# Kernel optimization log

Hardware: AMD Instinct MI355X
Metric: run time of the kernel (lower is better)

The kernel has to match this reference:

```python
import jax, jax.numpy as jnp
import numpy as np

N_NODES = 100000
IN_CH, HID_CH, OUT_CH = 128, 256, 128
N_EDGES = 1600000
N_LABEL = 200000


def setup_inputs() -> dict:
    key = jax.random.key(0)
    ks = jax.random.split(key, 9)
    x = jax.random.normal(ks[0], (N_NODES, IN_CH), dtype=jnp.float32)
    edge_index = jax.random.randint(ks[1], (2, N_EDGES), 0, N_NODES, dtype=jnp.int64)
    edge_label_index = jax.random.randint(ks[2], (2, N_LABEL), 0, N_NODES, dtype=jnp.int64)
    def glorot(k, fan_in, fan_out):
        s = jnp.sqrt(2.0 / (fan_in + fan_out))
        return jax.random.normal(k, (fan_in, fan_out), dtype=jnp.float32) * s
    # SAGEConv params: lin_l (aggregated neighbors, with bias), lin_r (root, no bias)
    Wl1 = glorot(ks[3], IN_CH, HID_CH)
    bl1 = jnp.zeros((HID_CH,), dtype=jnp.float32)
    Wr1 = glorot(ks[4], IN_CH, HID_CH)
    Wl2 = glorot(ks[5], HID_CH, OUT_CH)
    bl2 = jnp.zeros((OUT_CH,), dtype=jnp.float32)
    Wr2 = glorot(ks[6], HID_CH, OUT_CH)
    return {"x": x, "edge_index": edge_index, "edge_label_index": edge_label_index,
            "Wl1": Wl1, "bl1": bl1, "Wr1": Wr1, "Wl2": Wl2, "bl2": bl2, "Wr2": Wr2}


def _sage_conv(x, src, dst, Wl, bl, Wr):
    # mean aggregation of source-node messages onto destination nodes
    n = x.shape[0]
    agg = jax.ops.segment_sum(x[src], dst, num_segments=n)          # [N, d]
    deg = jax.ops.segment_sum(jnp.ones_like(dst, dtype=x.dtype), dst, num_segments=n)
    agg = agg / jnp.maximum(deg, 1.0)[:, None]
    return agg @ Wl + bl + x @ Wr


def reference(x, edge_index, edge_label_index, Wl1, bl1, Wr1, Wl2, bl2, Wr2):
    src, dst = edge_index[0], edge_index[1]
    h = jax.nn.relu(_sage_conv(x, src, dst, Wl1, bl1, Wr1))
    z = _sage_conv(h, src, dst, Wl2, bl2, Wr2)                      # [N, out]
    lsrc, ldst = edge_label_index[0], edge_label_index[1]
    return jnp.sum(z[lsrc] * z[ldst], axis=-1)                      # [E_label]
```

## Files before the change

### kernel.cpp

```cpp
#include <hip/hip_runtime.h>

#define N_NODES 100000
#define N_EDGES 1600000
#define N_LABEL 200000
#define C_IN 128
#define C_HID 256
#define C_OUT 128

#define BCHUNK 64
#define NBUCK ((N_NODES + BCHUNK - 1) / BCHUNK)
#define NBF 64
#define EPB (N_EDGES / NBF)
#define FLEN (NBUCK * NBF)
#define ESTORE 2048

typedef __attribute__((ext_vector_type(8))) short bf16x8;
typedef __attribute__((ext_vector_type(4))) float f32x4;

__device__ __forceinline__ ushort f2bf(float f) {
  uint u = __float_as_uint(f);
  return (ushort)((u + 0x7fffu + ((u >> 16) & 1u)) >> 16);
}

__device__ __forceinline__ float bfl(uint u) { return __uint_as_float(u << 16); }
__device__ __forceinline__ float bfh(uint u) {
  return __uint_as_float(u & 0xffff0000u);
}

__device__ __forceinline__ void async_copy16(const void* g, void* lds) {
  __builtin_amdgcn_global_load_lds((const __attribute__((address_space(1))) void*)g,
                                   (__attribute__((address_space(3))) void*)lds,
                                   16, 0, 0);
}

__global__ __launch_bounds__(256) void bucket_count(const int* __restrict__ dst,
                                                    int* __restrict__ cnt) {
  __shared__ int lcnt[NBUCK];
  const int t = threadIdx.x;
  const int base = blockIdx.x * EPB;
  for (int b = t; b < NBUCK; b += 256) lcnt[b] = 0;
  __syncthreads();
  for (int i = t; i < EPB; i += 256) {
    atomicAdd(&lcnt[dst[base + i] >> 6], 1);
  }
  __syncthreads();
  for (int b = t; b < NBUCK; b += 256) cnt[b * NBF + blockIdx.x] = lcnt[b];
}

template <int LEN>
__global__ __launch_bounds__(256) void scan_sums(const int* __restrict__ a,
                                                 int* __restrict__ bsum) {
  __shared__ int red[256];
  const int t = threadIdx.x;
  const int idx = blockIdx.x * 1024 + t * 4;
  int s = 0;
  if (idx + 3 < LEN) {
    const int4 v = *(const int4*)&a[idx];
    s = v.x + v.y + v.z + v.w;
  } else {
    for (int j = 0; j < 4 && idx + j < LEN; ++j) s += a[idx + j];
  }
  red[t] = s;
  __syncthreads();
  for (int off = 128; off > 0; off >>= 1) {
    if (t < off) red[t] += red[t + off];
    __syncthreads();
  }
  if (t == 0) bsum[blockIdx.x] = red[0];
}

__global__ __launch_bounds__(128) void scan_tops(const int* __restrict__ bsum,
                                                 int* __restrict__ bpre,
                                                 int* __restrict__ total, int nb) {
  __shared__ int sh[128];
  const int t = threadIdx.x;
  sh[t] = (t < nb) ? bsum[t] : 0;
  __syncthreads();
  for (int off = 1; off < 128; off <<= 1) {
    int v = 0;
    if (t >= off) v = sh[t - off];
    __syncthreads();
    if (t >= off) sh[t] += v;
    __syncthreads();
  }
  if (t < nb) bpre[t] = (t == 0) ? 0 : sh[t - 1];
  if (t == nb - 1) *total = sh[t];
}

template <int LEN>
__global__ __launch_bounds__(256) void scan_apply(int* __restrict__ a,
                                                  const int* __restrict__ bpre) {
  __shared__ int sh[256];
  const int t = threadIdx.x;
  const int idx = blockIdx.x * 1024 + t * 4;
  int4 v = make_int4(0, 0, 0, 0);
  const bool full = (idx + 3 < LEN);
  if (full) {
    v = *(const int4*)&a[idx];
  } else {
    if (idx + 0 < LEN) v.x = a[idx + 0];
    if (idx + 1 < LEN) v.y = a[idx + 1];
    if (idx + 2 < LEN) v.z = a[idx + 2];
    if (idx + 3 < LEN) v.w = a[idx + 3];
  }
  sh[t] = v.x + v.y + v.z + v.w;
  __syncthreads();
  for (int off = 1; off < 256; off <<= 1) {
    int u = 0;
    if (t >= off) u = sh[t - off];
    __syncthreads();
    if (t >= off) sh[t] += u;
    __syncthreads();
  }
  const int base = bpre[blockIdx.x] + ((t == 0) ? 0 : sh[t - 1]);
  int4 e;
  e.x = base;
  e.y = base + v.x;
  e.z = base + v.x + v.y;
  e.w = base + v.x + v.y + v.z;
  if (full) {
    *(int4*)&a[idx] = e;
  } else {
    if (idx + 0 < LEN) a[idx + 0] = e.x;
    if (idx + 1 < LEN) a[idx + 1] = e.y;
    if (idx + 2 < LEN) a[idx + 2] = e.z;
    if (idx + 3 < LEN) a[idx + 3] = e.w;
  }
}

__global__ __launch_bounds__(256) void bucket_fill(const int* __restrict__ src,
                                                   const int* __restrict__ dst,
                                                   const int* __restrict__ cnt,
                                                   uint* __restrict__ tmp) {
  __shared__ int lcur[NBUCK];
  const int t = threadIdx.x;
  const int base = blockIdx.x * EPB;
  for (int b = t; b < NBUCK; b += 256) lcur[b] = cnt[b * NBF + blockIdx.x];
  __syncthreads();
  for (int i = t; i < EPB; i += 256) {
    const int d = dst[base + i];
    const int s = src[base + i];
    const int pos = atomicAdd(&lcur[d >> 6], 1);
    tmp[pos] = ((uint)s << 6) | (uint)(d & 63);
  }
}

__global__ __launch_bounds__(256) void csr_build(const int* __restrict__ cnt,
                                                 uint* __restrict__ tmp,
                                                 int* __restrict__ row_start) {
  __shared__ uint est[ESTORE];
  __shared__ uint eso[ESTORE];
  __shared__ int lcnt[BCHUNK];
  __shared__ int lcur[BCHUNK];
  const int b = blockIdx.x;
  const int t = threadIdx.x;
  const int s = cnt[b * NBF];
  const int e = cnt[(b + 1) * NBF];
  const int n = e - s;
  for (int j = t; j < n; j += 256) est[j] = tmp[s + j];
  if (t < BCHUNK) lcnt[t] = 0;
  __syncthreads();
  for (int j = t; j < n; j += 256) atomicAdd(&lcnt[est[j] & 63], 1);
  __syncthreads();
  for (int off = 1; off < BCHUNK; off <<= 1) {
    int v = 0;
    if (t >= off && t < BCHUNK) v = lcnt[t - off];
    __syncthreads();
    if (t >= off && t < BCHUNK) lcnt[t] += v;
    __syncthreads();
  }
  if (t < BCHUNK) {
    const int ex = (t == 0) ? 0 : lcnt[t - 1];
    lcur[t] = ex;
    const int node = b * BCHUNK + t;
    if (node < N_NODES) row_start[node] = s + ex;
  }
  if (b == NBUCK - 1 && t == 0) row_start[N_NODES] = e;
  __syncthreads();
  for (int j = t; j < n; j += 256) {
    const uint v = est[j];
    const int pos = atomicAdd(&lcur[v & 63], 1);
    eso[pos] = v >> 6;
  }
  __syncthreads();
  for (int j = t; j < n; j += 256) tmp[s + j] = eso[j];
}

__global__ __launch_bounds__(256) void cast_bf16(const float* __restrict__ in,
                                                 ushort* __restrict__ out) {
  const size_t i = ((size_t)blockIdx.x * 256 + threadIdx.x) * 8;
  const float4 a = *(const float4*)&in[i];
  const float4 b = *(const float4*)&in[i + 4];
  uint4 o;
  o.x = (uint)f2bf(a.x) | ((uint)f2bf(a.y) << 16);
  o.y = (uint)f2bf(a.z) | ((uint)f2bf(a.w) << 16);
  o.z = (uint)f2bf(b.x) | ((uint)f2bf(b.y) << 16);
  o.w = (uint)f2bf(b.z) | ((uint)f2bf(b.w) << 16);
  *(uint4*)&out[i] = o;
}

__global__ __launch_bounds__(256) void prep_wt(const float* __restrict__ Wl1,
                                               const float* __restrict__ Wr1,
                                               const float* __restrict__ Wl2,
                                               const float* __restrict__ Wr2,
                                               ushort* __restrict__ WT1,
                                               ushort* __restrict__ WT2) {
  const int n = blockIdx.x;
  const int k = threadIdx.x;
  const float v1 = (k < 128) ? Wl1[k * 256 + n] : Wr1[(k - 128) * 256 + n];
  WT1[n * 256 + k] = f2bf(v1);
  const float v2 = (n < 128) ? Wl2[k * 128 + n] : Wr2[k * 128 + (n - 128)];
  WT2[n * 256 + k] = f2bf(v2);
}

template <int MODE>
__global__ __launch_bounds__(256) void gather_mean_b(const int* __restrict__ row_start,
                                                     const uint* __restrict__ csr_src,
                                                     const ushort* __restrict__ feat,
                                                     ushort* __restrict__ bout,
                                                     float* __restrict__ z) {
  const int wid = blockIdx.x * 4 + (threadIdx.x >> 6);
  const int lane = threadIdx.x & 63;
  if (wid >= N_NODES) return;
  const int s = row_start[wid];
  const int e = row_start[wid + 1];
  const int slot = lane >> 4;
  const int c0 = (lane & 15) * 8;
  float acc[8] = {};
  int j = s + slot;
#define ACC8(r)                                   \
  acc[0] += bfl(r.x); acc[1] += bfh(r.x);         \
  acc[2] += bfl(r.y); acc[3] += bfh(r.y);         \
  acc[4] += bfl(r.z); acc[5] += bfh(r.z);         \
  acc[6] += bfl(r.w); acc[7] += bfh(r.w);
  for (; j + 12 < e; j += 16) {
    const uint s0 = csr_src[j];
    const uint s1 = csr_src[j + 4];
    const uint s2 = csr_src[j + 8];
    const uint s3 = csr_src[j + 12];
    const uint4 r0 = *(const uint4*)&feat[(size_t)s0 * 128 + c0];
    const uint4 r1 = *(const uint4*)&feat[(size_t)s1 * 128 + c0];
    const uint4 r2 = *(const uint4*)&feat[(size_t)s2 * 128 + c0];
    const uint4 r3 = *(const uint4*)&feat[(size_t)s3 * 128 + c0];
    ACC8(r0) ACC8(r1) ACC8(r2) ACC8(r3)
  }
  for (; j < e; j += 4) {
    const uint s0 = csr_src[j];
    const uint4 r0 = *(const uint4*)&feat[(size_t)s0 * 128 + c0];
    ACC8(r0)
  }
#undef ACC8
#pragma unroll
  for (int k = 0; k < 8; ++k) {
    acc[k] += __shfl_xor(acc[k], 16, 64);
    acc[k] += __shfl_xor(acc[k], 32, 64);
  }
  if (slot == 0) {
    const float rd = 1.0f / fmaxf((float)(e - s), 1.0f);
    if (MODE == 0) {
      uint4 o;
      o.x = (uint)f2bf(acc[0] * rd) | ((uint)f2bf(acc[1] * rd) << 16);
      o.y = (uint)f2bf(acc[2] * rd) | ((uint)f2bf(acc[3] * rd) << 16);
      o.z = (uint)f2bf(acc[4] * rd) | ((uint)f2bf(acc[5] * rd) << 16);
      o.w = (uint)f2bf(acc[6] * rd) | ((uint)f2bf(acc[7] * rd) << 16);
      *(uint4*)&bout[(size_t)wid * 128 + c0] = o;
    } else {
      float4 z0 = *(const float4*)&z[(size_t)wid * 128 + c0];
      float4 z1 = *(const float4*)&z[(size_t)wid * 128 + c0 + 4];
      z0.x += acc[0] * rd; z0.y += acc[1] * rd;
      z0.z += acc[2] * rd; z0.w += acc[3] * rd;
      z1.x += acc[4] * rd; z1.y += acc[5] * rd;
      z1.z += acc[6] * rd; z1.w += acc[7] * rd;
      *(float4*)&z[(size_t)wid * 128 + c0] = z0;
      *(float4*)&z[(size_t)wid * 128 + c0 + 4] = z1;
    }
  }
}

__global__ __launch_bounds__(256) void gemm_fused(const ushort* __restrict__ aggb,
                                                  const ushort* __restrict__ xb,
                                                  const ushort* __restrict__ WT1,
                                                  const ushort* __restrict__ WT2,
                                                  const float* __restrict__ bl1,
                                                  const float* __restrict__ bl2,
                                                  ushort* __restrict__ p,
                                                  float* __restrict__ zp) {
  __shared__ ushort As[2][2048];
  __shared__ ushort Bs[2][8192];
  __shared__ ushort Ht[64 * 256];
  const int tid = threadIdx.x;
  const int w = tid >> 6;
  const int l = tid & 63;
  const int row0 = blockIdx.x * 64;
  const int wn = w * 64;
  const int fr = l & 15;
  const int kg16 = (l >> 4) * 16;
  const int cr = (l >> 4) * 4;
  const int cc = l & 15;

  const int arow = tid >> 2;
  const int akb = (tid & 3) * 16;
  const int akbs = akb ^ (((arow >> 1) & 3) << 4);
  int agr = row0 + arow;
  agr = (agr < N_NODES) ? agr : (N_NODES - 1);
  const int brow_l = l >> 2;
  const int bkb = (l & 3) * 16;

#define STAGE(buf, kc)                                                        \
  {                                                                           \
    const ushort* Ab_ = ((kc) < 4) ? aggb : xb;                               \
    async_copy16((const char*)Ab_ + (size_t)agr * 256 + ((kc)&3) * 64 + akbs, \
                 (char*)As[buf] + w * 1024);                                  \
    _Pragma("unroll") for (int i_ = 0; i_ < 4; ++i_) {                        \
      const int c_ = w * 4 + i_;                                              \
      const int n_ = c_ * 16 + brow_l;                                        \
      const int kbs_ = bkb ^ (((n_ >> 1) & 3) << 4);                          \
      async_copy16((const char*)WT1 + (size_t)n_ * 512 + (kc)*64 + kbs_,      \
                   (char*)Bs[buf] + c_ * 1024);                               \
    }                                                                         \
  }

  {
    f32x4 acc[4][4] = {};
    STAGE(0, 0)
    __syncthreads();
    int cur = 0;
#pragma unroll
    for (int kc = 0; kc < 8; ++kc) {
      if (kc < 7) STAGE(cur ^ 1, kc + 1)
      bf16x8 af[4], bfr[4];
#pragma unroll
      for (int i = 0; i < 4; ++i) {
        const int ra = i * 16 + fr;
        const int ba = ra * 64 + (kg16 ^ (((ra >> 1) & 3) << 4));
        af[i] = *(const bf16x8*)((const char*)As[cur] + ba);
      }
#pragma unroll
      for (int j = 0; j < 4; ++j) {
        const int nb = wn + j * 16 + fr;
        const int bb = nb * 64 + (kg16 ^ (((nb >> 1) & 3) << 4));
        bfr[j] = *(const bf16x8*)((const char*)Bs[cur] + bb);
      }
#pragma unroll
      for (int i = 0; i < 4; ++i)
#pragma unroll
        for (int j = 0; j < 4; ++j)
          acc[i][j] = __builtin_amdgcn_mfma_f32_16x16x32_bf16(af[i], bfr[j],
                                                              acc[i][j], 0, 0, 0);
      __syncthreads();
      cur ^= 1;
    }
#pragma unroll
    for (int i = 0; i < 4; ++i) {
#pragma unroll
      for (int j = 0; j < 4; ++j) {
        const int col = wn + j * 16 + cc;
        const float bv = bl1[col];
#pragma unroll
        for (int r = 0; r < 4; ++r) {
          const int row = i * 16 + cr + r;
          const float v = fmaxf(acc[i][j][r] + bv, 0.f);
          const int ba = (row * 512 + col * 2) ^ ((row & 7) << 4);
          *(ushort*)((char*)Ht + ba) = f2bf(v);
        }
      }
    }
  }
#undef STAGE
  __syncthreads();

  f32x4 acc2[4][4] = {};
#pragma unroll
  for (int kc = 0; kc < 8; ++kc) {
    bf16x8 af[4], bfr[4];
#pragma unroll
    for (int i = 0; i < 4; ++i) {
      const int row = i * 16 + fr;
      const int ba = (row * 512 + kc * 64 + kg16) ^ ((row & 7) << 4);
      af[i] = *(const bf16x8*)((const char*)Ht + ba);
    }
#pragma unroll
    for (int j = 0; j < 4; ++j) {
      const int n = wn + j * 16 + fr;
      bfr[j] = *(const bf16x8*)((const char*)WT2 + (size_t)n * 512 + kc * 64 +
                                kg16);
    }
#pragma unroll
    for (int i = 0; i < 4; ++i)
#pragma unroll
      for (int j = 0; j < 4; ++j)
        acc2[i][j] = __builtin_amdgcn_mfma_f32_16x16x32_bf16(af[i], bfr[j],
                                                             acc2[i][j], 0, 0, 0);
  }
#pragma unroll
  for (int i = 0; i < 4; ++i) {
#pragma unroll
    for (int j = 0; j < 4; ++j) {
      const int col = wn + j * 16 + cc;
      const int gcl = col & 127;
      const bool is_p = (col < 128);
      const float bv = is_p ? 0.f : bl2[gcl];
#pragma unroll
      for (int r = 0; r < 4; ++r) {
        const int grow = row0 + i * 16 + cr + r;
        if (grow < N_NODES) {
          const float v = acc2[i][j][r] + bv;
          if (is_p)
            p[(size_t)grow * 128 + gcl] = f2bf(v);
          else
            zp[(size_t)grow * 128 + gcl] = v;
        }
      }
    }
  }
}

__global__ __launch_bounds__(256) void dot_kernel(const int* __restrict__ ls,
                                                  const int* __restrict__ ld,
                                                  const float* __restrict__ z,
                                                  float* __restrict__ out) {
  long long tid = (long long)blockIdx.x * 256 + threadIdx.x;
  int e = (int)(tid >> 5);
  int lane = (int)(tid & 31);
  if (e >= N_LABEL) return;
  int a = ls[e], b = ld[e];
  const float4 va = *(const float4*)&z[(size_t)a * 128 + lane * 4];
  const float4 vb = *(const float4*)&z[(size_t)b * 128 + lane * 4];
  float p = va.x * vb.x + va.y * vb.y + va.z * vb.z + va.w * vb.w;
  p += __shfl_xor(p, 16, 32);
  p += __shfl_xor(p, 8, 32);
  p += __shfl_xor(p, 4, 32);
  p += __shfl_xor(p, 2, 32);
  p += __shfl_xor(p, 1, 32);
  if (lane == 0) out[e] = p;
}

extern "C" void kernel_launch(void* const* d_in, const int* in_sizes, int n_in,
                              void* d_out, int out_size, void* d_ws, size_t ws_size,
                              hipStream_t stream) {
  const float* x = (const float*)d_in[0];
  const int* ei = (const int*)d_in[1];
  const int* eli = (const int*)d_in[2];
  const float* Wl1 = (const float*)d_in[3];
  const float* bl1 = (const float*)d_in[4];
  const float* Wr1 = (const float*)d_in[5];
  const float* Wl2 = (const float*)d_in[6];
  const float* bl2 = (const float*)d_in[7];
  const float* Wr2 = (const float*)d_in[8];
  float* out = (float*)d_out;

  const int* e_src = ei;
  const int* e_dst = ei + N_EDGES;
  const int* l_src = eli;
  const int* l_dst = eli + N_LABEL;

  char* ws = (char*)d_ws;
  ushort* xb = (ushort*)(ws + 0);
  ushort* aggb = (ushort*)(ws + 25600000);
  ushort* p = (ushort*)(ws + 102400000);
  float* z = (float*)(ws + 128000000);
  ushort* WT1 = (ushort*)(ws + 179200000);
  ushort* WT2 = (ushort*)(ws + 179331072);
  uint* tmp = (uint*)(ws + 179462144);
  int* cnt = (int*)(ws + 185862144);
  int* bsum = (int*)(ws + 186270000);
  int* bpre = bsum + 128;
  int* row_start = (int*)(ws + 186280000);

  const int SBLK = (FLEN + 1023) / 1024;

  bucket_count<<<NBF, 256, 0, stream>>>(e_dst, cnt);
  scan_sums<FLEN><<<SBLK, 256, 0, stream>>>(cnt, bsum);
  scan_tops<<<1, 128, 0, stream>>>(bsum, bpre, &cnt[FLEN], SBLK);
  scan_apply<FLEN><<<SBLK, 256, 0, stream>>>(cnt, bpre);
  bucket_fill<<<NBF, 256, 0, stream>>>(e_src, e_dst, cnt, tmp);
  csr_build<<<NBUCK, 256, 0, stream>>>(cnt, tmp, row_start);

  cast_bf16<<<(N_NODES * C_IN) / (256 * 8), 256, 0, stream>>>(x, xb);
  prep_wt<<<256, 256, 0, stream>>>(Wl1, Wr1, Wl2, Wr2, WT1, WT2);

  gather_mean_b<0><<<(N_NODES + 3) / 4, 256, 0, stream>>>(row_start, tmp, xb,
                                                          aggb, nullptr);
  gemm_fused<<<(N_NODES + 63) / 64, 256, 0, stream>>>(aggb, xb, WT1, WT2, bl1,
                                                      bl2, p, z);
  gather_mean_b<1><<<(N_NODES + 3) / 4, 256, 0, stream>>>(row_start, tmp, p,
                                                          nullptr, z);

  dot_kernel<<<(int)(((long long)N_LABEL * 32) / 256), 256, 0, stream>>>(
      l_src, l_dst, z, out);
}
```

Measured before the change: 348.0 us.

## Merge prep kernels, fold scan tops into apply, single-buffer GEMM staging

```diff
diff --git a/kernel.cpp b/kernel.cpp
--- a/kernel.cpp
+++ b/kernel.cpp
@@ -13,6 +13,8 @@
 #define EPB (N_EDGES / NBF)
 #define FLEN (NBUCK * NBF)
 #define ESTORE 2048
+#define CAST_NB ((N_NODES * C_IN) / (256 * 8))
+#define SBLK ((FLEN + 1023) / 1024)
 
 typedef __attribute__((ext_vector_type(8))) short bf16x8;
 typedef __attribute__((ext_vector_type(4))) float f32x4;
@@ -33,32 +35,59 @@
                                    16, 0, 0);
 }
 
-__global__ __launch_bounds__(256) void bucket_count(const int* __restrict__ dst,
-                                                    int* __restrict__ cnt) {
+__global__ __launch_bounds__(256) void prep_kernel(const int* __restrict__ dst,
+                                                   int* __restrict__ cnt,
+                                                   const float* __restrict__ Wl1,
+                                                   const float* __restrict__ Wr1,
+                                                   const float* __restrict__ Wl2,
+                                                   const float* __restrict__ Wr2,
+                                                   ushort* __restrict__ WT1,
+                                                   ushort* __restrict__ WT2,
+                                                   const float* __restrict__ x,
+                                                   ushort* __restrict__ xb) {
   __shared__ int lcnt[NBUCK];
+  const int blk = blockIdx.x;
   const int t = threadIdx.x;
-  const int base = blockIdx.x * EPB;
-  for (int b = t; b < NBUCK; b += 256) lcnt[b] = 0;
-  __syncthreads();
-  for (int i = t; i < EPB; i += 256) {
-    atomicAdd(&lcnt[dst[base + i] >> 6], 1);
-  }
-  __syncthreads();
-  for (int b = t; b < NBUCK; b += 256) cnt[b * NBF + blockIdx.x] = lcnt[b];
-}
-
-template <int LEN>
+  if (blk < NBF) {
+    const int base = blk * EPB;
+    for (int b = t; b < NBUCK; b += 256) lcnt[b] = 0;
+    __syncthreads();
+    for (int i = t; i < EPB; i += 256) {
+      atomicAdd(&lcnt[dst[base + i] >> 6], 1);
+    }
+    __syncthreads();
+    for (int b = t; b < NBUCK; b += 256) cnt[b * NBF + blk] = lcnt[b];
+  } else if (blk < NBF + 256) {
+    const int n = blk - NBF;
+    const int k = t;
+    const float v1 = (k < 128) ? Wl1[k * 256 + n] : Wr1[(k - 128) * 256 + n];
+    WT1[n * 256 + k] = f2bf(v1);
+    const float v2 = (n < 128) ? Wl2[k * 128 + n] : Wr2[k * 128 + (n - 128)];
+    WT2[n * 256 + k] = f2bf(v2);
+  } else {
+    const size_t i = ((size_t)(blk - NBF - 256) * 256 + t) * 8;
+    const float4 a = *(const float4*)&x[i];
+    const float4 b = *(const float4*)&x[i + 4];
+    uint4 o;
+    o.x = (uint)f2bf(a.x) | ((uint)f2bf(a.y) << 16);
+    o.y = (uint)f2bf(a.z) | ((uint)f2bf(a.w) << 16);
+    o.z = (uint)f2bf(b.x) | ((uint)f2bf(b.y) << 16);
+    o.w = (uint)f2bf(b.z) | ((uint)f2bf(b.w) << 16);
+    *(uint4*)&xb[i] = o;
+  }
+}
+
 __global__ __launch_bounds__(256) void scan_sums(const int* __restrict__ a,
                                                  int* __restrict__ bsum) {
   __shared__ int red[256];
   const int t = threadIdx.x;
   const int idx = blockIdx.x * 1024 + t * 4;
   int s = 0;
-  if (idx + 3 < LEN) {
+  if (idx + 3 < FLEN) {
     const int4 v = *(const int4*)&a[idx];
     s = v.x + v.y + v.z + v.w;
   } else {
-    for (int j = 0; j < 4 && idx + j < LEN; ++j) s += a[idx + j];
+    for (int j = 0; j < 4 && idx + j < FLEN; ++j) s += a[idx + j];
   }
   red[t] = s;
   __syncthreads();
@@ -69,39 +98,33 @@
   if (t == 0) bsum[blockIdx.x] = red[0];
 }
 
-__global__ __launch_bounds__(128) void scan_tops(const int* __restrict__ bsum,
-                                                 int* __restrict__ bpre,
-                                                 int* __restrict__ total, int nb) {
-  __shared__ int sh[128];
+__global__ __launch_bounds__(256) void scan_apply(int* __restrict__ a,
+                                                  const int* __restrict__ bsum) {
+  __shared__ int sh[256];
+  __shared__ int bsc[128];
   const int t = threadIdx.x;
-  sh[t] = (t < nb) ? bsum[t] : 0;
+  if (t < 128) bsc[t] = (t < SBLK) ? bsum[t] : 0;
   __syncthreads();
   for (int off = 1; off < 128; off <<= 1) {
     int v = 0;
-    if (t >= off) v = sh[t - off];
-    __syncthreads();
-    if (t >= off) sh[t] += v;
-    __syncthreads();
-  }
-  if (t < nb) bpre[t] = (t == 0) ? 0 : sh[t - 1];
-  if (t == nb - 1) *total = sh[t];
-}
-
-template <int LEN>
-__global__ __launch_bounds__(256) void scan_apply(int* __restrict__ a,
-                                                  const int* __restrict__ bpre) {
-  __shared__ int sh[256];
-  const int t = threadIdx.x;
+    if (t < 128 && t >= off) v = bsc[t - off];
+    __syncthreads();
+    if (t < 128 && t >= off) bsc[t] += v;
+    __syncthreads();
+  }
+  const int bbase = (blockIdx.x == 0) ? 0 : bsc[blockIdx.x - 1];
+  if (blockIdx.x == SBLK - 1 && t == 0) a[FLEN] = bsc[SBLK - 1];
+
   const int idx = blockIdx.x * 1024 + t * 4;
   int4 v = make_int4(0, 0, 0, 0);
-  const bool full = (idx + 3 < LEN);
+  const bool full = (idx + 3 < FLEN);
   if (full) {
     v = *(const int4*)&a[idx];
   } else {
-    if (idx + 0 < LEN) v.x = a[idx + 0];
-    if (idx + 1 < LEN) v.y = a[idx + 1];
-    if (idx + 2 < LEN) v.z = a[idx + 2];
-    if (idx + 3 < LEN) v.w = a[idx + 3];
+    if (idx + 0 < FLEN) v.x = a[idx + 0];
+    if (idx + 1 < FLEN) v.y = a[idx + 1];
+    if (idx + 2 < FLEN) v.z = a[idx + 2];
+    if (idx + 3 < FLEN) v.w = a[idx + 3];
   }
   sh[t] = v.x + v.y + v.z + v.w;
   __syncthreads();
@@ -112,7 +135,7 @@
     if (t >= off) sh[t] += u;
     __syncthreads();
   }
-  const int base = bpre[blockIdx.x] + ((t == 0) ? 0 : sh[t - 1]);
+  const int base = bbase + ((t == 0) ? 0 : sh[t - 1]);
   int4 e;
   e.x = base;
   e.y = base + v.x;
@@ -121,10 +144,10 @@
   if (full) {
     *(int4*)&a[idx] = e;
   } else {
-    if (idx + 0 < LEN) a[idx + 0] = e.x;
-    if (idx + 1 < LEN) a[idx + 1] = e.y;
-    if (idx + 2 < LEN) a[idx + 2] = e.z;
-    if (idx + 3 < LEN) a[idx + 3] = e.w;
+    if (idx + 0 < FLEN) a[idx + 0] = e.x;
+    if (idx + 1 < FLEN) a[idx + 1] = e.y;
+    if (idx + 2 < FLEN) a[idx + 2] = e.z;
+    if (idx + 3 < FLEN) a[idx + 3] = e.w;
   }
 }
 
@@ -184,33 +207,6 @@
   }
   __syncthreads();
   for (int j = t; j < n; j += 256) tmp[s + j] = eso[j];
-}
-
-__global__ __launch_bounds__(256) void cast_bf16(const float* __restrict__ in,
-                                                 ushort* __restrict__ out) {
-  const size_t i = ((size_t)blockIdx.x * 256 + threadIdx.x) * 8;
-  const float4 a = *(const float4*)&in[i];
-  const float4 b = *(const float4*)&in[i + 4];
-  uint4 o;
-  o.x = (uint)f2bf(a.x) | ((uint)f2bf(a.y) << 16);
-  o.y = (uint)f2bf(a.z) | ((uint)f2bf(a.w) << 16);
-  o.z = (uint)f2bf(b.x) | ((uint)f2bf(b.y) << 16);
-  o.w = (uint)f2bf(b.z) | ((uint)f2bf(b.w) << 16);
-  *(uint4*)&out[i] = o;
-}
-
-__global__ __launch_bounds__(256) void prep_wt(const float* __restrict__ Wl1,
-                                               const float* __restrict__ Wr1,
-                                               const float* __restrict__ Wl2,
-                                               const float* __restrict__ Wr2,
-                                               ushort* __restrict__ WT1,
-                                               ushort* __restrict__ WT2) {
-  const int n = blockIdx.x;
-  const int k = threadIdx.x;
-  const float v1 = (k < 128) ? Wl1[k * 256 + n] : Wr1[(k - 128) * 256 + n];
-  WT1[n * 256 + k] = f2bf(v1);
-  const float v2 = (n < 128) ? Wl2[k * 128 + n] : Wr2[k * 128 + (n - 128)];
-  WT2[n * 256 + k] = f2bf(v2);
 }
 
 template <int MODE>
@@ -285,8 +281,8 @@
                                                   const float* __restrict__ bl2,
                                                   ushort* __restrict__ p,
                                                   float* __restrict__ zp) {
-  __shared__ ushort As[2][2048];
-  __shared__ ushort Bs[2][8192];
+  __shared__ ushort As[2048];
+  __shared__ ushort Bs[8192];
   __shared__ ushort Ht[64 * 256];
   const int tid = threadIdx.x;
   const int w = tid >> 6;
@@ -306,40 +302,34 @@
   const int brow_l = l >> 2;
   const int bkb = (l & 3) * 16;
 
-#define STAGE(buf, kc)                                                        \
-  {                                                                           \
-    const ushort* Ab_ = ((kc) < 4) ? aggb : xb;                               \
-    async_copy16((const char*)Ab_ + (size_t)agr * 256 + ((kc)&3) * 64 + akbs, \
-                 (char*)As[buf] + w * 1024);                                  \
-    _Pragma("unroll") for (int i_ = 0; i_ < 4; ++i_) {                        \
-      const int c_ = w * 4 + i_;                                              \
-      const int n_ = c_ * 16 + brow_l;                                        \
-      const int kbs_ = bkb ^ (((n_ >> 1) & 3) << 4);                          \
-      async_copy16((const char*)WT1 + (size_t)n_ * 512 + (kc)*64 + kbs_,      \
-                   (char*)Bs[buf] + c_ * 1024);                               \
-    }                                                                         \
-  }
-
   {
     f32x4 acc[4][4] = {};
-    STAGE(0, 0)
-    __syncthreads();
-    int cur = 0;
-#pragma unroll
     for (int kc = 0; kc < 8; ++kc) {
-      if (kc < 7) STAGE(cur ^ 1, kc + 1)
+      const ushort* Ab = (kc < 4) ? aggb : xb;
+      __syncthreads();
+      async_copy16((const char*)Ab + (size_t)agr * 256 + (kc & 3) * 64 + akbs,
+                   (char*)As + w * 1024);
+#pragma unroll
+      for (int i_ = 0; i_ < 4; ++i_) {
+        const int c_ = w * 4 + i_;
+        const int n_ = c_ * 16 + brow_l;
+        const int kbs_ = bkb ^ (((n_ >> 1) & 3) << 4);
+        async_copy16((const char*)WT1 + (size_t)n_ * 512 + kc * 64 + kbs_,
+                     (char*)Bs + c_ * 1024);
+      }
+      __syncthreads();
       bf16x8 af[4], bfr[4];
 #pragma unroll
       for (int i = 0; i < 4; ++i) {
         const int ra = i * 16 + fr;
         const int ba = ra * 64 + (kg16 ^ (((ra >> 1) & 3) << 4));
-        af[i] = *(const bf16x8*)((const char*)As[cur] + ba);
+        af[i] = *(const bf16x8*)((const char*)As + ba);
       }
 #pragma unroll
       for (int j = 0; j < 4; ++j) {
         const int nb = wn + j * 16 + fr;
         const int bb = nb * 64 + (kg16 ^ (((nb >> 1) & 3) << 4));
-        bfr[j] = *(const bf16x8*)((const char*)Bs[cur] + bb);
+        bfr[j] = *(const bf16x8*)((const char*)Bs + bb);
       }
 #pragma unroll
       for (int i = 0; i < 4; ++i)
@@ -347,8 +337,6 @@
         for (int j = 0; j < 4; ++j)
           acc[i][j] = __builtin_amdgcn_mfma_f32_16x16x32_bf16(af[i], bfr[j],
                                                               acc[i][j], 0, 0, 0);
-      __syncthreads();
-      cur ^= 1;
     }
 #pragma unroll
     for (int i = 0; i < 4; ++i) {
@@ -366,7 +354,6 @@
       }
     }
   }
-#undef STAGE
   __syncthreads();
 
   f32x4 acc2[4][4] = {};
@@ -464,20 +451,14 @@
   uint* tmp = (uint*)(ws + 179462144);
   int* cnt = (int*)(ws + 185862144);
   int* bsum = (int*)(ws + 186270000);
-  int* bpre = bsum + 128;
   int* row_start = (int*)(ws + 186280000);
 
-  const int SBLK = (FLEN + 1023) / 1024;
-
-  bucket_count<<<NBF, 256, 0, stream>>>(e_dst, cnt);
-  scan_sums<FLEN><<<SBLK, 256, 0, stream>>>(cnt, bsum);
-  scan_tops<<<1, 128, 0, stream>>>(bsum, bpre, &cnt[FLEN], SBLK);
-  scan_apply<FLEN><<<SBLK, 256, 0, stream>>>(cnt, bpre);
+  prep_kernel<<<NBF + 256 + CAST_NB, 256, 0, stream>>>(
+      e_dst, cnt, Wl1, Wr1, Wl2, Wr2, WT1, WT2, x, xb);
+  scan_sums<<<SBLK, 256, 0, stream>>>(cnt, bsum);
+  scan_apply<<<SBLK, 256, 0, stream>>>(cnt, bsum);
   bucket_fill<<<NBF, 256, 0, stream>>>(e_src, e_dst, cnt, tmp);
   csr_build<<<NBUCK, 256, 0, stream>>>(cnt, tmp, row_start);
-
-  cast_bf16<<<(N_NODES * C_IN) / (256 * 8), 256, 0, stream>>>(x, xb);
-  prep_wt<<<256, 256, 0, stream>>>(Wl1, Wr1, Wl2, Wr2, WT1, WT2);
 
   gather_mean_b<0><<<(N_NODES + 3) / 4, 256, 0, stream>>>(row_start, tmp, xb,
                                                           aggb, nullptr);
```

Result: faster. 325.1 us (-6.6%).
